# Kernel optimization log

Hardware: AMD Instinct MI355X
Metric: run time of the kernel (lower is better)

Reference implementation:

```python
import jax, jax.numpy as jnp
import numpy as np

N, E, S = 20000, 160000, 3        # nodes, edges, message-passing steps
L, NODE_D, EDGE_D, OUT = 128, 12, 7, 3
LN_EPS = 1e-5


def _mlp(x, W0, b0, W1, b1, W2, b2):
    # Linear -> ReLU -> Linear -> ReLU -> Linear (widths: in->L->L->out)
    h = jax.nn.relu(x @ W0 + b0)
    h = jax.nn.relu(h @ W1 + b1)
    return h @ W2 + b2


def _ln(h, g, b):
    mu = jnp.mean(h, axis=-1, keepdims=True)
    var = jnp.mean((h - mu) ** 2, axis=-1, keepdims=True)
    return (h - mu) * jax.lax.rsqrt(var + LN_EPS) * g + b


def setup_inputs() -> dict:
    ks = iter(jax.random.split(jax.random.key(0), 64))
    w = lambda *s: jax.random.normal(next(ks), s, jnp.float32) * 0.05
    z = lambda *s: jnp.zeros(s, jnp.float32)
    o = lambda *s: jnp.ones(s, jnp.float32)
    inp = {
        'node_x': jax.random.normal(next(ks), (N, NODE_D), jnp.float32),
        'edge_x': jax.random.normal(next(ks), (E, EDGE_D), jnp.float32),
        'enc_n_W0': w(NODE_D, L), 'enc_n_b0': z(L), 'enc_n_W1': w(L, L), 'enc_n_b1': z(L),
        'enc_n_W2': w(L, L), 'enc_n_b2': z(L), 'enc_n_g': o(L), 'enc_n_be': z(L),
        'enc_e_W0': w(EDGE_D, L), 'enc_e_b0': z(L), 'enc_e_W1': w(L, L), 'enc_e_b1': z(L),
        'enc_e_W2': w(L, L), 'enc_e_b2': z(L), 'enc_e_g': o(L), 'enc_e_be': z(L),
        'gnb_e_W0': w(S, 3 * L, L), 'gnb_e_b0': z(S, L), 'gnb_e_W1': w(S, L, L), 'gnb_e_b1': z(S, L),
        'gnb_e_W2': w(S, L, L), 'gnb_e_b2': z(S, L), 'gnb_e_g': o(S, L), 'gnb_e_be': z(S, L),
        'gnb_n_W0': w(S, 2 * L, L), 'gnb_n_b0': z(S, L), 'gnb_n_W1': w(S, L, L), 'gnb_n_b1': z(S, L),
        'gnb_n_W2': w(S, L, L), 'gnb_n_b2': z(S, L), 'gnb_n_g': o(S, L), 'gnb_n_be': z(S, L),
        'dec_W0': w(L, L), 'dec_b0': z(L), 'dec_W1': w(L, L), 'dec_b1': z(L),
        'dec_W2': w(L, OUT), 'dec_b2': z(OUT),
        'senders': jax.random.randint(next(ks), (E,), 0, N, jnp.int32),
        'receivers': jax.random.randint(next(ks), (E,), 0, N, jnp.int32),
    }
    return inp


def reference(node_x, edge_x,
              enc_n_W0, enc_n_b0, enc_n_W1, enc_n_b1, enc_n_W2, enc_n_b2, enc_n_g, enc_n_be,
              enc_e_W0, enc_e_b0, enc_e_W1, enc_e_b1, enc_e_W2, enc_e_b2, enc_e_g, enc_e_be,
              gnb_e_W0, gnb_e_b0, gnb_e_W1, gnb_e_b1, gnb_e_W2, gnb_e_b2, gnb_e_g, gnb_e_be,
              gnb_n_W0, gnb_n_b0, gnb_n_W1, gnb_n_b1, gnb_n_W2, gnb_n_b2, gnb_n_g, gnb_n_be,
              dec_W0, dec_b0, dec_W1, dec_b1, dec_W2, dec_b2,
              senders, receivers):
    num_nodes = node_x.shape[0]
    # Encoder: MLP + LayerNorm on nodes and edges
    nf = _ln(_mlp(node_x, enc_n_W0, enc_n_b0, enc_n_W1, enc_n_b1, enc_n_W2, enc_n_b2), enc_n_g, enc_n_be)
    ef = _ln(_mlp(edge_x, enc_e_W0, enc_e_b0, enc_e_W1, enc_e_b1, enc_e_W2, enc_e_b2), enc_e_g, enc_e_be)

    def step(carry, p):
        nf, ef = carry
        (eW0, eb0, eW1, eb1, eW2, eb2, eg, ebe,
         nW0, nb0, nW1, nb1, nW2, nb2, ng, nbe) = p
        # gather sender/receiver node features -> concat with edge features -> edge MLP
        cat_e = jnp.concatenate([nf[senders], nf[receivers], ef], axis=-1)  # [E, 3L]
        new_ef = _ln(_mlp(cat_e, eW0, eb0, eW1, eb1, eW2, eb2), eg, ebe)
        # scatter-sum updated edge features to receiver nodes
        agg = jax.ops.segment_sum(new_ef, receivers, num_segments=num_nodes)  # [N, L]
        new_nf = _ln(_mlp(jnp.concatenate([nf, agg], axis=-1), nW0, nb0, nW1, nb1, nW2, nb2), ng, nbe)
        # residual connections on both nodes and edges
        return (nf + new_nf, ef + new_ef), None

    step_params = (gnb_e_W0, gnb_e_b0, gnb_e_W1, gnb_e_b1, gnb_e_W2, gnb_e_b2, gnb_e_g, gnb_e_be,
                   gnb_n_W0, gnb_n_b0, gnb_n_W1, gnb_n_b1, gnb_n_W2, gnb_n_b2, gnb_n_g, gnb_n_be)
    (nf, ef), _ = jax.lax.scan(step, (nf, ef), step_params)

    # Decoder: MLP without LayerNorm
    return _mlp(nf, dec_W0, dec_b0, dec_W1, dec_b1, dec_W2, dec_b2)
```

## Files before the change

### kernel.cpp

```cpp
#include <hip/hip_runtime.h>
#include <hip/hip_bf16.h>

#define NN 20000
#define EE 160000

typedef __attribute__((ext_vector_type(8))) short bf16x8;
typedef __attribute__((ext_vector_type(4))) float f32x4;

__device__ __forceinline__ unsigned short f2bf(float f) {
    unsigned int u = __float_as_uint(f);
    u += 0x7FFFu + ((u >> 16) & 1);
    return (unsigned short)(u >> 16);
}
__device__ __forceinline__ float bf2f(short s) {
    return __uint_as_float(((unsigned int)(unsigned short)s) << 16);
}
__device__ __forceinline__ bf16x8 pack8(float4 a, float4 b) {
    bf16x8 r;
    r[0] = (short)f2bf(a.x); r[1] = (short)f2bf(a.y);
    r[2] = (short)f2bf(a.z); r[3] = (short)f2bf(a.w);
    r[4] = (short)f2bf(b.x); r[5] = (short)f2bf(b.y);
    r[6] = (short)f2bf(b.z); r[7] = (short)f2bf(b.w);
    return r;
}

#define SH_STRIDE 136
#define SW_STRIDE 56
#define SH64 132
#define SW64 72

__device__ __forceinline__ void bar_lgkm() {
    asm volatile("s_waitcnt lgkmcnt(0)\n\ts_barrier" ::: "memory");
}

__device__ __forceinline__ void mfma_sweep_lds(f32x4 (&acc)[2][8], bf16x8 a0, bf16x8 a1,
                                               const short* sWb, int lm, int lq)
{
#pragma unroll
    for (int ct = 0; ct < 8; ++ct) {
        bf16x8 b = *(const bf16x8*)(sWb + (ct * 16 + lm) * SW_STRIDE + lq * 8);
        acc[0][ct] = __builtin_amdgcn_mfma_f32_16x16x32_bf16(a0, b, acc[0][ct], 0, 0, 0);
        acc[1][ct] = __builtin_amdgcn_mfma_f32_16x16x32_bf16(a1, b, acc[1][ct], 0, 0, 0);
    }
}

__device__ __forceinline__ void mfma_sweep64(f32x4 (&acc)[2][8], bf16x8 a0, bf16x8 a1,
                                             const short* sWb, int colOff, int lm)
{
#pragma unroll
    for (int ct = 0; ct < 8; ++ct) {
        bf16x8 b = *(const bf16x8*)(sWb + (ct * 16 + lm) * SW64 + colOff);
        acc[0][ct] = __builtin_amdgcn_mfma_f32_16x16x32_bf16(a0, b, acc[0][ct], 0, 0, 0);
        acc[1][ct] = __builtin_amdgcn_mfma_f32_16x16x32_bf16(a1, b, acc[1][ct], 0, 0, 0);
    }
}

__device__ __forceinline__ void mfma_sweepNS(f32x4 (&acc)[4], bf16x8 a,
                                             const short* sWb, int ch, int colOff, int lm)
{
#pragma unroll
    for (int i = 0; i < 4; ++i) {
        int ct = ch * 4 + i;
        bf16x8 b = *(const bf16x8*)(sWb + (ct * 16 + lm) * SW64 + colOff);
        acc[i] = __builtin_amdgcn_mfma_f32_16x16x32_bf16(a, b, acc[i], 0, 0, 0);
    }
}

template<int NT>
struct WStage { bf16x8 v[512 / NT]; };

template<int NT>
__device__ __forceinline__ void wload(WStage<NT>& ws, const short* __restrict__ Wt,
                                      int Kpad, int k0, int tid)
{
#pragma unroll
    for (int j = 0; j < 256 / NT; ++j) {
        int i = tid + j * NT;
        int r = i >> 1, h = i & 1;
        const short* src = Wt + (size_t)r * Kpad + k0 + h * 16;
        ws.v[2 * j]     = *(const bf16x8*)src;
        ws.v[2 * j + 1] = *(const bf16x8*)(src + 8);
    }
}
template<int NT>
__device__ __forceinline__ void wstore(const WStage<NT>& ws, short* __restrict__ sW, int tid)
{
#pragma unroll
    for (int j = 0; j < 256 / NT; ++j) {
        int i = tid + j * NT;
        int r = i >> 1, h = i & 1;
        short* dst = sW + r * SW_STRIDE + h * 16;
        *(bf16x8*)dst       = ws.v[2 * j];
        *(bf16x8*)(dst + 8) = ws.v[2 * j + 1];
    }
}

struct WStage64 { bf16x8 v[4]; };
__device__ __forceinline__ void wload64(WStage64& ws, const short* __restrict__ Wt,
                                        int Kpad, int k0, int tid)
{
#pragma unroll
    for (int j = 0; j < 4; ++j) {
        int i = tid + j * 256;
        int r = i >> 3, h = i & 7;
        ws.v[j] = *(const bf16x8*)(Wt + (size_t)r * Kpad + k0 + h * 8);
    }
}
__device__ __forceinline__ void wstore64(const WStage64& ws, short* __restrict__ sW, int tid)
{
#pragma unroll
    for (int j = 0; j < 4; ++j) {
        int i = tid + j * 256;
        int r = i >> 3, h = i & 7;
        *(bf16x8*)(sW + r * SW64 + h * 8) = ws.v[j];
    }
}

__device__ __forceinline__ void zero_acc(f32x4 (&acc)[2][8]) {
#pragma unroll
    for (int i = 0; i < 2; ++i)
#pragma unroll
        for (int j = 0; j < 8; ++j) acc[i][j] = (f32x4)(0.f);
}

__device__ __forceinline__ void park(const f32x4 (&acc)[2][8], const float* __restrict__ bias,
                                     short* __restrict__ sH, int w32, int lm, int lq)
{
#pragma unroll
    for (int ct = 0; ct < 8; ++ct) {
        float bb = bias[ct * 16 + lm];
#pragma unroll
        for (int rt = 0; rt < 2; ++rt) {
            int rbase = w32 + rt * 16 + lq * 4;
#pragma unroll
            for (int reg = 0; reg < 4; ++reg) {
                float v = fmaxf(acc[rt][ct][reg] + bb, 0.f);
                sH[(rbase + reg) * SH_STRIDE + ct * 16 + lm] = (short)f2bf(v);
            }
        }
    }
}

__device__ __forceinline__ void parkNS(const f32x4 (&acc)[4], const float* __restrict__ bias,
                                       short* __restrict__ sH, int g16, int ch, int lm, int lq)
{
#pragma unroll
    for (int i = 0; i < 4; ++i) {
        int ct = ch * 4 + i;
        float bb = bias[ct * 16 + lm];
#pragma unroll
        for (int reg = 0; reg < 4; ++reg) {
            float v = fmaxf(acc[i][reg] + bb, 0.f);
            sH[(g16 + lq * 4 + reg) * SH_STRIDE + ct * 16 + lm] = (short)f2bf(v);
        }
    }
}

__device__ __forceinline__ void park64(const f32x4 (&acc)[2][8], const float* __restrict__ bias,
                                       short* __restrict__ sH, int w32, int lm, int lq)
{
#pragma unroll
    for (int ct = 0; ct < 8; ++ct) {
        float bb = bias[ct * 16 + lm];
#pragma unroll
        for (int rt = 0; rt < 2; ++rt) {
            int rbase = w32 + rt * 16 + lq * 4;
#pragma unroll
            for (int reg = 0; reg < 4; ++reg) {
                float v = fmaxf(acc[rt][ct][reg] + bb, 0.f);
                sH[(rbase + reg) * SH64 + ct * 16 + lm] = (short)f2bf(v);
            }
        }
    }
}

struct Frag {
    bf16x8 a0, a1;
    float4 f0, f1, f2, f3;
    int isF;
};

template<int MODE>
__device__ __forceinline__ void load_frag(Frag& fr, int c,
    const short* __restrict__ nfb, const float* __restrict__ aggf,
    int r0m, int r1m, const short* sH, int w32, int lm, int lq)
{
    int kq = lq * 8;
    fr.isF = 0;
    if (MODE == 0) {
        fr.a0 = *(const bf16x8*)&sH[(w32 + lm) * SH_STRIDE + c * 32 + kq];
        fr.a1 = *(const bf16x8*)&sH[(w32 + 16 + lm) * SH_STRIDE + c * 32 + kq];
    } else if (MODE == 2) {
        int seg = c >> 2, kb = (c & 3) * 32 + kq;
        if (seg == 0) {
            fr.a0 = *(const bf16x8*)(nfb + (size_t)r0m * 128 + kb);
            fr.a1 = *(const bf16x8*)(nfb + (size_t)r1m * 128 + kb);
        } else {
            const float* p0 = aggf + (size_t)r0m * 128 + kb;
            const float* p1 = aggf + (size_t)r1m * 128 + kb;
            fr.f0 = *(const float4*)p0; fr.f1 = *(const float4*)(p0 + 4);
            fr.f2 = *(const float4*)p1; fr.f3 = *(const float4*)(p1 + 4);
            fr.isF = 1;
        }
    } else {
        int kb = c * 32 + kq;
        fr.a0 = *(const bf16x8*)(nfb + (size_t)r0m * 128 + kb);
        fr.a1 = *(const bf16x8*)(nfb + (size_t)r1m * 128 + kb);
    }
}

template<int MODE>
__device__ __forceinline__ void load_fragNS(Frag& fr, int c,
    const short* __restrict__ nfb, const float* __restrict__ aggf, int r0m, int lq)
{
    fr.isF = 0;
    if (MODE == 2 && c >= 2) {
        const float* p = aggf + (size_t)r0m * 128 + (c - 2) * 64 + lq * 8;
        fr.f0 = *(const float4*)p;        fr.f1 = *(const float4*)(p + 4);
        fr.f2 = *(const float4*)(p + 32); fr.f3 = *(const float4*)(p + 36);
        fr.isF = 1;
    } else {
        const short* p = nfb + (size_t)r0m * 128 + c * 64 + lq * 8;
        fr.a0 = *(const bf16x8*)p;
        fr.a1 = *(const bf16x8*)(p + 32);
    }
}

struct Frag64 { bf16x8 a[4]; };

__device__ __forceinline__ void load_frag64(Frag64& fr, int c,
    const short* __restrict__ nfb, const short* __restrict__ efHi,
    int iS0, int iS1, int iR0, int iR1, size_t eO0, size_t eO1, int lq)
{
    int kb = (c & 1) * 64 + lq * 8;
    int seg = c >> 1;
    const short *base0, *base1;
    if (seg == 0)      { base0 = nfb + (size_t)iS0 * 128; base1 = nfb + (size_t)iS1 * 128; }
    else if (seg == 1) { base0 = nfb + (size_t)iR0 * 128; base1 = nfb + (size_t)iR1 * 128; }
    else               { base0 = efHi + eO0;              base1 = efHi + eO1; }
    fr.a[0] = *(const bf16x8*)(base0 + kb);
    fr.a[1] = *(const bf16x8*)(base1 + kb);
    fr.a[2] = *(const bf16x8*)(base0 + kb + 32);
    fr.a[3] = *(const bf16x8*)(base1 + kb + 32);
}

template<int RESID>
__global__ __launch_bounds__(256) void gnn_edge64(
    const short* __restrict__ Wt0,
    const short* __restrict__ Wt1, const short* __restrict__ Wt2,
    const float* __restrict__ b0, const float* __restrict__ b1, const float* __restrict__ b2,
    const float* __restrict__ g, const float* __restrict__ be,
    const short* __restrict__ nfb,
    short* __restrict__ efHi, short* __restrict__ efLo,
    const int* __restrict__ eList,
    const int* __restrict__ senders, const int* __restrict__ receivers,
    float* __restrict__ aggOut)
{
    __shared__ short sH[128 * SH64];
    __shared__ short sW[128 * SW64];
    __shared__ int sRcv[128], sSnd[128];
    const int tid = threadIdx.x;
    const int lane = tid & 63;
    const int w = tid >> 6;
    const int lm = lane & 15;
    const int lq = lane >> 4;
    const int w32 = w * 32;
    const int m0 = blockIdx.x * 128;

    if (tid < 128) {
        int slot = m0 + tid;
        int e = eList ? eList[slot] : slot;
        sRcv[tid] = receivers[e];
        sSnd[tid] = senders[e];
    }
    bar_lgkm();

    f32x4 acc[2][8];
    zero_acc(acc);

    const int s0 = w32 + 2 * lm, s1 = s0 + 1;
    const int iS0 = sSnd[s0], iS1 = sSnd[s1];
    const int iR0 = sRcv[s0], iR1 = sRcv[s1];
    const size_t eO0 = (size_t)(m0 + s0) * 128;
    const size_t eO1 = (size_t)(m0 + s1) * 128;

    {
        WStage64 ws, wsn;
        Frag64 cur, nxt;
        wload64(ws, Wt0, 384, 0, tid);
        load_frag64(cur, 0, nfb, efHi, iS0, iS1, iR0, iR1, eO0, eO1, lq);
#pragma unroll
        for (int c = 0; c < 6; ++c) {
            if (c + 1 < 6) {
                wload64(wsn, Wt0, 384, (c + 1) * 64, tid);
                load_frag64(nxt, c + 1, nfb, efHi, iS0, iS1, iR0, iR1, eO0, eO1, lq);
            }
            bar_lgkm();
            wstore64(ws, sW, tid);
            bar_lgkm();
            mfma_sweep64(acc, cur.a[0], cur.a[1], sW, lq * 8, lm);
            mfma_sweep64(acc, cur.a[2], cur.a[3], sW, 32 + lq * 8, lm);
            ws = wsn; cur = nxt;
        }
    }
    bar_lgkm();
    park64(acc, b0, sH, w32, lm, lq);

    zero_acc(acc);
    {
        WStage64 ws, wsn;
        wload64(ws, Wt1, 128, 0, tid);
#pragma unroll
        for (int c = 0; c < 2; ++c) {
            if (c == 0) wload64(wsn, Wt1, 128, 64, tid);
            bf16x8 a0h0 = *(const bf16x8*)&sH[(w32 + lm) * SH64 + c * 64 + lq * 8];
            bf16x8 a1h0 = *(const bf16x8*)&sH[(w32 + 16 + lm) * SH64 + c * 64 + lq * 8];
            bf16x8 a0h1 = *(const bf16x8*)&sH[(w32 + lm) * SH64 + c * 64 + 32 + lq * 8];
            bf16x8 a1h1 = *(const bf16x8*)&sH[(w32 + 16 + lm) * SH64 + c * 64 + 32 + lq * 8];
            bar_lgkm();
            wstore64(ws, sW, tid);
            bar_lgkm();
            mfma_sweep64(acc, a0h0, a1h0, sW, lq * 8, lm);
            mfma_sweep64(acc, a0h1, a1h1, sW, 32 + lq * 8, lm);
            ws = wsn;
        }
    }
    bar_lgkm();
    park64(acc, b1, sH, w32, lm, lq);

    zero_acc(acc);
    {
        WStage64 ws, wsn;
        wload64(ws, Wt2, 128, 0, tid);
#pragma unroll
        for (int c = 0; c < 2; ++c) {
            if (c == 0) wload64(wsn, Wt2, 128, 64, tid);
            bf16x8 a0h0 = *(const bf16x8*)&sH[(w32 + lm) * SH64 + c * 64 + lq * 8];
            bf16x8 a1h0 = *(const bf16x8*)&sH[(w32 + 16 + lm) * SH64 + c * 64 + lq * 8];
            bf16x8 a0h1 = *(const bf16x8*)&sH[(w32 + lm) * SH64 + c * 64 + 32 + lq * 8];
            bf16x8 a1h1 = *(const bf16x8*)&sH[(w32 + 16 + lm) * SH64 + c * 64 + 32 + lq * 8];
            bar_lgkm();
            wstore64(ws, sW, tid);
            bar_lgkm();
            mfma_sweep64(acc, a0h0, a1h0, sW, lq * 8, lm);
            mfma_sweep64(acc, a0h1, a1h1, sW, 32 + lq * 8, lm);
            ws = wsn;
        }
    }

    float g_[8], be_[8], b2_[8];
#pragma unroll
    for (int ct = 0; ct < 8; ++ct) {
        g_[ct] = g[ct * 16 + lm]; be_[ct] = be[ct * 16 + lm]; b2_[ct] = b2[ct * 16 + lm];
    }
    float run[8];
    int curRcv = -1;
#pragma unroll
    for (int j = 0; j < 8; ++j) {
        int rt = j & 1, reg = j >> 1;
        int rloc = w32 + lq * 8 + j;
        float v[8];
        float s = 0.f;
#pragma unroll
        for (int ct = 0; ct < 8; ++ct) { v[ct] = acc[rt][ct][reg] + b2_[ct]; s += v[ct]; }
        s += __shfl_xor(s, 1); s += __shfl_xor(s, 2);
        s += __shfl_xor(s, 4); s += __shfl_xor(s, 8);
        float mu = s * (1.f / 128.f);
        float q = 0.f;
#pragma unroll
        for (int ct = 0; ct < 8; ++ct) { v[ct] -= mu; q += v[ct] * v[ct]; }
        q += __shfl_xor(q, 1); q += __shfl_xor(q, 2);
        q += __shfl_xor(q, 4); q += __shfl_xor(q, 8);
        float rs = rsqrtf(q * (1.f / 128.f) + 1e-5f);
        int rcv = sRcv[rloc];
        float o[8];
#pragma unroll
        for (int ct = 0; ct < 8; ++ct) {
            o[ct] = v[ct] * rs * g_[ct] + be_[ct];
            if (RESID) {
                size_t gi = (size_t)(m0 + rloc) * 128 + ct * 16 + lm;
                float x = bf2f(efHi[gi]) + bf2f(efLo[gi]) + o[ct];
                short h = (short)f2bf(x);
                efHi[gi] = h;
                efLo[gi] = (short)f2bf(x - bf2f(h));
            }
        }
        if (rcv != curRcv) {
            if (curRcv >= 0) {
#pragma unroll
                for (int ct = 0; ct < 8; ++ct)
                    atomicAdd(aggOut + (size_t)curRcv * 128 + ct * 16 + lm, run[ct]);
            }
            curRcv = rcv;
#pragma unroll
            for (int ct = 0; ct < 8; ++ct) run[ct] = o[ct];
        } else {
#pragma unroll
            for (int ct = 0; ct < 8; ++ct) run[ct] += o[ct];
        }
    }
    if (curRcv >= 0) {
#pragma unroll
        for (int ct = 0; ct < 8; ++ct)
            atomicAdd(aggOut + (size_t)curRcv * 128 + ct * 16 + lm, run[ct]);
    }
}

template<int NW, int MODE, int PAIR>
__global__ __launch_bounds__(NW * 64) void gnn_mlp(
    const short* __restrict__ Wt0,
    const short* __restrict__ Wt1, const short* __restrict__ Wt2,
    const float* __restrict__ b0, const float* __restrict__ b1, const float* __restrict__ b2,
    const float* __restrict__ g, const float* __restrict__ be,
    const float* __restrict__ A0f, int K0,
    const short* __restrict__ nfb,
    const float* __restrict__ aggf,
    const int* __restrict__ eList,
    float* __restrict__ outF, short* __restrict__ outB, short* __restrict__ outB2,
    float* __restrict__ aggOut,
    float* __restrict__ decOut,
    int M, int resid)
{
    constexpr int KP0 = (MODE == 2) ? 256 : (MODE == 3) ? 128 : 32;
    constexpr int nC0 = KP0 / 32;
    __shared__ short sH[NW * 32 * SH_STRIDE];
    __shared__ short sW[128 * SW_STRIDE];
    const int tid = threadIdx.x;
    const int lane = tid & 63;
    const int w = tid >> 6;
    const int lm = lane & 15;
    const int lq = lane >> 4;
    const int w32 = w * 32;
    const int m0 = blockIdx.x * (NW * 32);
    constexpr int NT = NW * 64;

    f32x4 acc[2][8];
    zero_acc(acc);

    if (MODE == 0) {
#pragma unroll
        for (int i = 0; i < 16; ++i) {
            int flat = lane + i * 64;
            int r = flat >> 5, k = flat & 31;
            int row = m0 + w32 + r;
            float v = 0.f;
            if (k < K0 && row < M) {
                int src = eList ? eList[row] : row;
                v = A0f[(size_t)src * K0 + k];
            }
            sH[(w32 + r) * SH_STRIDE + k] = (short)f2bf(v);
        }
    }
    const int r0m = min(m0 + w32 + lm, M - 1);
    const int r1m = min(m0 + w32 + 16 + lm, M - 1);

    {
        WStage<NT> ws, wsn;
        Frag cur, nx1, nx2;
        wload<NT>(ws, Wt0, KP0, 0, tid);
        load_frag<MODE>(cur, 0, nfb, aggf, r0m, r1m, sH, w32, lm, lq);
        if (nC0 > 1)
            load_frag<MODE>(nx1, 1, nfb, aggf, r0m, r1m, sH, w32, lm, lq);
#pragma unroll
        for (int c = 0; c < nC0; ++c) {
            if (c + 1 < nC0)
                wload<NT>(wsn, Wt0, KP0, (c + 1) * 32, tid);
            if (c + 2 < nC0)
                load_frag<MODE>(nx2, c + 2, nfb, aggf, r0m, r1m, sH, w32, lm, lq);
            bar_lgkm();
            wstore<NT>(ws, sW, tid);
            bar_lgkm();
            bf16x8 u0, u1;
            if (cur.isF) { u0 = pack8(cur.f0, cur.f1); u1 = pack8(cur.f2, cur.f3); }
            else         { u0 = cur.a0;               u1 = cur.a1; }
            mfma_sweep_lds(acc, u0, u1, sW, lm, lq);
            ws = wsn; cur = nx1; nx1 = nx2;
        }
    }
    bar_lgkm();
    park(acc, b0, sH, w32, lm, lq);

    zero_acc(acc);
    {
        WStage<NT> ws, wsn;
        wload<NT>(ws, Wt1, 128, 0, tid);
#pragma unroll
        for (int c = 0; c < 4; ++c) {
            if (c + 1 < 4) wload<NT>(wsn, Wt1, 128, (c + 1) * 32, tid);
            bf16x8 a0 = *(const bf16x8*)&sH[(w32 + lm) * SH_STRIDE + c * 32 + lq * 8];
            bf16x8 a1 = *(const bf16x8*)&sH[(w32 + 16 + lm) * SH_STRIDE + c * 32 + lq * 8];
            bar_lgkm();
            wstore<NT>(ws, sW, tid);
            bar_lgkm();
            mfma_sweep_lds(acc, a0, a1, sW, lm, lq);
            ws = wsn;
        }
    }
    bar_lgkm();
    park(acc, b1, sH, w32, lm, lq);

    zero_acc(acc);
    {
        WStage<NT> ws, wsn;
        wload<NT>(ws, Wt2, 128, 0, tid);
#pragma unroll
        for (int c = 0; c < 4; ++c) {
            if (c + 1 < 4) wload<NT>(wsn, Wt2, 128, (c + 1) * 32, tid);
            bf16x8 a0 = *(const bf16x8*)&sH[(w32 + lm) * SH_STRIDE + c * 32 + lq * 8];
            bf16x8 a1 = *(const bf16x8*)&sH[(w32 + 16 + lm) * SH_STRIDE + c * 32 + lq * 8];
            bar_lgkm();
            wstore<NT>(ws, sW, tid);
            bar_lgkm();
            mfma_sweep_lds(acc, a0, a1, sW, lm, lq);
            ws = wsn;
        }
    }

    float g_[8], be_[8], b2_[8];
#pragma unroll
    for (int ct = 0; ct < 8; ++ct) {
        g_[ct] = g[ct * 16 + lm]; be_[ct] = be[ct * 16 + lm]; b2_[ct] = b2[ct * 16 + lm];
    }
#pragma unroll
    for (int rt = 0; rt < 2; ++rt) {
#pragma unroll
        for (int reg = 0; reg < 4; ++reg) {
            int row = m0 + w32 + rt * 16 + lq * 4 + reg;
            float v[8];
            float s = 0.f;
#pragma unroll
            for (int ct = 0; ct < 8; ++ct) { v[ct] = acc[rt][ct][reg] + b2_[ct]; s += v[ct]; }
            s += __shfl_xor(s, 1); s += __shfl_xor(s, 2);
            s += __shfl_xor(s, 4); s += __shfl_xor(s, 8);
            float mu = s * (1.f / 128.f);
            float q = 0.f;
#pragma unroll
            for (int ct = 0; ct < 8; ++ct) { v[ct] -= mu; q += v[ct] * v[ct]; }
            q += __shfl_xor(q, 1); q += __shfl_xor(q, 2);
            q += __shfl_xor(q, 4); q += __shfl_xor(q, 8);
            float rs = rsqrtf(q * (1.f / 128.f) + 1e-5f);
            if (row < M) {
#pragma unroll
                for (int ct = 0; ct < 8; ++ct) {
                    float o = v[ct] * rs * g_[ct] + be_[ct];
                    size_t gi = (size_t)row * 128 + ct * 16 + lm;
                    if (PAIR) {
                        short h = (short)f2bf(o);
                        outB[gi]  = h;
                        outB2[gi] = (short)f2bf(o - bf2f(h));
                    } else {
                        if (resid) {
                            float ns = outF[gi] + o;
                            outF[gi] = ns;
                            if (outB) outB[gi] = (short)f2bf(ns);
                        } else {
                            outF[gi] = o;
                            if (outB) outB[gi] = (short)f2bf(o);
                        }
                    }
                }
            }
        }
    }
}

template<int MODE>
__global__ __launch_bounds__(256) void gnn_mlpNS(
    const short* __restrict__ Wt0,
    const short* __restrict__ Wt1, const short* __restrict__ Wt2,
    const float* __restrict__ b0, const float* __restrict__ b1, const float* __restrict__ b2,
    const float* __restrict__ g, const float* __restrict__ be,
    const float* __restrict__ A0f, int K0,
    const short* __restrict__ nfb,
    const float* __restrict__ aggf,
    float* __restrict__ outF, short* __restrict__ outB,
    float* __restrict__ aggOut,
    float* __restrict__ decOut,
    int M, int resid)
{
    __shared__ short sH[32 * SH_STRIDE];
    __shared__ short sW[128 * SW64];
    __shared__ float sX[2][32];
    __shared__ float sY[2][32];
    const int tid = threadIdx.x;
    const int lane = tid & 63;
    const int w = tid >> 6;
    const int gidx = w >> 1;
    const int ch = w & 1;
    const int lm = lane & 15;
    const int lq = lane >> 4;
    const int g16 = gidx * 16;
    const int m0 = blockIdx.x * 32;
    const int r0m = min(m0 + g16 + lm, M - 1);

    f32x4 acc[4];
#pragma unroll
    for (int i = 0; i < 4; ++i) acc[i] = (f32x4)(0.f);

    if (MODE == 0) {
#pragma unroll
        for (int i = 0; i < 4; ++i) {
            int flat = tid + i * 256;
            int r = flat >> 5, k = flat & 31;
            int row = m0 + r;
            float v = (k < K0 && row < M) ? A0f[(size_t)row * K0 + k] : 0.f;
            sH[r * SH_STRIDE + k] = (short)f2bf(v);
        }
        {
            const short* src = Wt0 + (size_t)(tid >> 1) * 32 + (tid & 1) * 16;
            bf16x8 w0 = *(const bf16x8*)src;
            bf16x8 w1 = *(const bf16x8*)(src + 8);
            bar_lgkm();
            short* dst = sW + (tid >> 1) * SW64 + (tid & 1) * 16;
            *(bf16x8*)dst       = w0;
            *(bf16x8*)(dst + 8) = w1;
            bar_lgkm();
        }
        bf16x8 a0 = *(const bf16x8*)&sH[(g16 + lm) * SH_STRIDE + lq * 8];
        mfma_sweepNS(acc, a0, sW, ch, lq * 8, lm);
    } else {
        constexpr int KP0 = (MODE == 2) ? 256 : 128;
        constexpr int nC0 = KP0 / 64;
        WStage64 ws, wsn;
        Frag cur, nxt;
        wload64(ws, Wt0, KP0, 0, tid);
        load_fragNS<MODE>(cur, 0, nfb, aggf, r0m, lq);
#pragma unroll
        for (int c = 0; c < nC0; ++c) {
            if (c + 1 < nC0) {
                wload64(wsn, Wt0, KP0, (c + 1) * 64, tid);
                load_fragNS<MODE>(nxt, c + 1, nfb, aggf, r0m, lq);
            }
            bar_lgkm();
            wstore64(ws, sW, tid);
            bar_lgkm();
            bf16x8 u0, u1;
            if (cur.isF) { u0 = pack8(cur.f0, cur.f1); u1 = pack8(cur.f2, cur.f3); }
            else         { u0 = cur.a0;                u1 = cur.a1; }
            mfma_sweepNS(acc, u0, sW, ch, lq * 8, lm);
            mfma_sweepNS(acc, u1, sW, ch, 32 + lq * 8, lm);
            ws = wsn; cur = nxt;
        }
    }
    bar_lgkm();
    parkNS(acc, b0, sH, g16, ch, lm, lq);
    bar_lgkm();

    if (MODE == 2 && aggOut) {
#pragma unroll
        for (int i = 0; i < 4; ++i) {
            int idx = tid + i * 256;
            int r = idx >> 5, c4 = idx & 31;
            int row = m0 + r;
            if (row < M)
                *(float4*)(aggOut + (size_t)row * 128 + c4 * 4) = make_float4(0.f, 0.f, 0.f, 0.f);
        }
    }

#pragma unroll
    for (int i = 0; i < 4; ++i) acc[i] = (f32x4)(0.f);
    {
        WStage64 ws, wsn;
        wload64(ws, Wt1, 128, 0, tid);
#pragma unroll
        for (int c = 0; c < 2; ++c) {
            if (c == 0) wload64(wsn, Wt1, 128, 64, tid);
            bf16x8 a0 = *(const bf16x8*)&sH[(g16 + lm) * SH_STRIDE + c * 64 + lq * 8];
            bf16x8 a1 = *(const bf16x8*)&sH[(g16 + lm) * SH_STRIDE + c * 64 + 32 + lq * 8];
            bar_lgkm();
            wstore64(ws, sW, tid);
            bar_lgkm();
            mfma_sweepNS(acc, a0, sW, ch, lq * 8, lm);
            mfma_sweepNS(acc, a1, sW, ch, 32 + lq * 8, lm);
            ws = wsn;
        }
    }
    bar_lgkm();
    parkNS(acc, b1, sH, g16, ch, lm, lq);
    bar_lgkm();

    if (MODE == 3) {
        if (tid < 96) {
            int r = tid / 3, o = tid - r * 3;
            int row = m0 + r;
            if (row < M) {
                float s = b2[o];
#pragma unroll
                for (int kk = 0; kk < 16; ++kk) {
                    bf16x8 h8 = *(const bf16x8*)&sH[r * SH_STRIDE + kk * 8];
#pragma unroll
                    for (int j = 0; j < 8; ++j)
                        s += bf2f(h8[j]) * A0f[(kk * 8 + j) * 3 + o];
                }
                decOut[(size_t)row * 3 + o] = s;
            }
        }
        return;
    }

#pragma unroll
    for (int i = 0; i < 4; ++i) acc[i] = (f32x4)(0.f);
    {
        WStage64 ws, wsn;
        wload64(ws, Wt2, 128, 0, tid);
#pragma unroll
        for (int c = 0; c < 2; ++c) {
            if (c == 0) wload64(wsn, Wt2, 128, 64, tid);
            bf16x8 a0 = *(const bf16x8*)&sH[(g16 + lm) * SH_STRIDE + c * 64 + lq * 8];
            bf16x8 a1 = *(const bf16x8*)&sH[(g16 + lm) * SH_STRIDE + c * 64 + 32 + lq * 8];
            bar_lgkm();
            wstore64(ws, sW, tid);
            bar_lgkm();
            mfma_sweepNS(acc, a0, sW, ch, lq * 8, lm);
            mfma_sweepNS(acc, a1, sW, ch, 32 + lq * 8, lm);
            ws = wsn;
        }
    }

    float g_[4], be_[4], b2_[4];
#pragma unroll
    for (int i = 0; i < 4; ++i) {
        int ct = ch * 4 + i;
        g_[i] = g[ct * 16 + lm]; be_[i] = be[ct * 16 + lm]; b2_[i] = b2[ct * 16 + lm];
    }
    float v[4][4], mu[4], rs_[4];
#pragma unroll
    for (int reg = 0; reg < 4; ++reg) {
        float s = 0.f;
#pragma unroll
        for (int i = 0; i < 4; ++i) { v[i][reg] = acc[i][reg] + b2_[i]; s += v[i][reg]; }
        s += __shfl_xor(s, 1); s += __shfl_xor(s, 2);
        s += __shfl_xor(s, 4); s += __shfl_xor(s, 8);
        if (lm == 0) sX[ch][g16 + lq * 4 + reg] = s;
    }
    bar_lgkm();
#pragma unroll
    for (int reg = 0; reg < 4; ++reg)
        mu[reg] = (sX[0][g16 + lq * 4 + reg] + sX[1][g16 + lq * 4 + reg]) * (1.f / 128.f);
#pragma unroll
    for (int reg = 0; reg < 4; ++reg) {
        float q = 0.f;
#pragma unroll
        for (int i = 0; i < 4; ++i) { v[i][reg] -= mu[reg]; q += v[i][reg] * v[i][reg]; }
        q += __shfl_xor(q, 1); q += __shfl_xor(q, 2);
        q += __shfl_xor(q, 4); q += __shfl_xor(q, 8);
        if (lm == 0) sY[ch][g16 + lq * 4 + reg] = q;
    }
    bar_lgkm();
#pragma unroll
    for (int reg = 0; reg < 4; ++reg)
        rs_[reg] = rsqrtf((sY[0][g16 + lq * 4 + reg] + sY[1][g16 + lq * 4 + reg]) * (1.f / 128.f) + 1e-5f);
#pragma unroll
    for (int reg = 0; reg < 4; ++reg) {
        int row = m0 + g16 + lq * 4 + reg;
        if (row < M) {
#pragma unroll
            for (int i = 0; i < 4; ++i) {
                float o = v[i][reg] * rs_[reg] * g_[i] + be_[i];
                size_t gi = (size_t)row * 128 + (size_t)(ch * 4 + i) * 16 + lm;
                if (resid) {
                    float ns = outF[gi] + o;
                    outF[gi] = ns;
                    if (outB) outB[gi] = (short)f2bf(ns);
                } else {
                    outF[gi] = o;
                    if (outB) outB[gi] = (short)f2bf(o);
                }
            }
        }
    }
}

__global__ void zero_i(int* __restrict__ p, int n)
{
    int i = blockIdx.x * 256 + threadIdx.x;
    if (i < n) p[i] = 0;
}
__global__ void csr_count(const int* __restrict__ recv, int* __restrict__ cnt, int E)
{
    int i = blockIdx.x * 256 + threadIdx.x;
    if (i < E) atomicAdd(&cnt[recv[i]], 1);
}
__global__ __launch_bounds__(256) void csr_scan(const int* __restrict__ cnt,
                                                int* __restrict__ cursor, int N)
{
    __shared__ int ssum[257];
    const int tid = threadIdx.x;
    const int per = (N + 255) / 256;
    const int lo = tid * per, hi = min(lo + per, N);
    int s = 0;
    for (int i = lo; i < hi; ++i) s += cnt[i];
    ssum[tid] = s;
    __syncthreads();
    if (tid == 0) {
        int run = 0;
        for (int i = 0; i < 256; ++i) { int t = ssum[i]; ssum[i] = run; run += t; }
        ssum[256] = run;
    }
    __syncthreads();
    int run = ssum[tid];
    for (int i = lo; i < hi; ++i) { int c = cnt[i]; cursor[i] = run; run += c; }
}
__global__ void csr_fill(const int* __restrict__ recv, int* __restrict__ cursor,
                         int* __restrict__ eList, int E)
{
    int i = blockIdx.x * 256 + threadIdx.x;
    if (i < E) {
        int pos = atomicAdd(&cursor[recv[i]], 1);
        eList[pos] = i;
    }
}

struct WtPrep { const float* src; int K; int Kpad; int dstOff; };
struct WtPrepAll { WtPrep m[26]; };

__global__ void wt_prep_kernel(WtPrepAll all, short* __restrict__ dst)
{
    const WtPrep p = all.m[blockIdx.y];
    int total = 128 * p.Kpad;
    int idx = blockIdx.x * 256 + threadIdx.x;
    if (idx >= total) return;
    int n = idx / p.Kpad, k = idx - n * p.Kpad;
    float v = (k < p.K) ? p.src[(size_t)k * 128 + n] : 0.f;
    dst[p.dstOff + idx] = (short)f2bf(v);
}

__global__ void zero_kernel(float4* __restrict__ p, long n4)
{
    long i = (long)blockIdx.x * blockDim.x + threadIdx.x;
    if (i < n4) p[i] = make_float4(0.f, 0.f, 0.f, 0.f);
}

extern "C" void kernel_launch(void* const* d_in, const int* in_sizes, int n_in,
                              void* d_out, int out_size, void* d_ws, size_t ws_size,
                              hipStream_t stream)
{
    const float* node_x   = (const float*)d_in[0];
    const float* edge_x   = (const float*)d_in[1];
    const float* enc_n_W0 = (const float*)d_in[2];
    const float* enc_n_b0 = (const float*)d_in[3];
    const float* enc_n_W1 = (const float*)d_in[4];
    const float* enc_n_b1 = (const float*)d_in[5];
    const float* enc_n_W2 = (const float*)d_in[6];
    const float* enc_n_b2 = (const float*)d_in[7];
    const float* enc_n_g  = (const float*)d_in[8];
    const float* enc_n_be = (const float*)d_in[9];
    const float* enc_e_W0 = (const float*)d_in[10];
    const float* enc_e_b0 = (const float*)d_in[11];
    const float* enc_e_W1 = (const float*)d_in[12];
    const float* enc_e_b1 = (const float*)d_in[13];
    const float* enc_e_W2 = (const float*)d_in[14];
    const float* enc_e_b2 = (const float*)d_in[15];
    const float* enc_e_g  = (const float*)d_in[16];
    const float* enc_e_be = (const float*)d_in[17];
    const float* gnb_e_W0 = (const float*)d_in[18];
    const float* gnb_e_b0 = (const float*)d_in[19];
    const float* gnb_e_W1 = (const float*)d_in[20];
    const float* gnb_e_b1 = (const float*)d_in[21];
    const float* gnb_e_W2 = (const float*)d_in[22];
    const float* gnb_e_b2 = (const float*)d_in[23];
    const float* gnb_e_g  = (const float*)d_in[24];
    const float* gnb_e_be = (const float*)d_in[25];
    const float* gnb_n_W0 = (const float*)d_in[26];
    const float* gnb_n_b0 = (const float*)d_in[27];
    const float* gnb_n_W1 = (const float*)d_in[28];
    const float* gnb_n_b1 = (const float*)d_in[29];
    const float* gnb_n_W2 = (const float*)d_in[30];
    const float* gnb_n_b2 = (const float*)d_in[31];
    const float* gnb_n_g  = (const float*)d_in[32];
    const float* gnb_n_be = (const float*)d_in[33];
    const float* dec_W0   = (const float*)d_in[34];
    const float* dec_b0   = (const float*)d_in[35];
    const float* dec_W1   = (const float*)d_in[36];
    const float* dec_b1   = (const float*)d_in[37];
    const float* dec_W2   = (const float*)d_in[38];
    const float* dec_b2   = (const float*)d_in[39];
    const int*   senders  = (const int*)d_in[40];
    const int*   receivers= (const int*)d_in[41];
    float* out = (float*)d_out;

    const int N = NN, E = EE;
    const int WT_TOTAL = (32 + 128 + 128 + 32 + 128 + 128 + 3 * (384 + 128 + 128 + 256 + 128 + 128)
                          + 128 + 128) * 128;

    float* nf   = (float*)d_ws;
    float* agg  = nf + (size_t)N * 128;
    short* efHi = (short*)(agg + (size_t)N * 128);
    short* efLo = efHi + (size_t)E * 128;
    short* nfbf = efLo + (size_t)E * 128;
    short* wt   = nfbf + (size_t)N * 128;
    int*   eList = (int*)(wt + WT_TOTAL);
    size_t need_sorted = (size_t)((char*)(eList + E) - (char*)d_ws);
    int* cnt    = (int*)agg;
    int* cursor = cnt + N;

    const bool useSorted = (ws_size >= need_sorted);
    const int* eL = useSorted ? eList : nullptr;

    WtPrepAll tbl;
    int nMat = 0, off = 0;
    int o_encn[3], o_ence[3], o_ge0[3], o_ge1[3], o_ge2[3], o_gn0[3], o_gn1[3], o_gn2[3], o_dec[2];
    auto add = [&](const float* src, int K, int Kpad) {
        tbl.m[nMat].src = src; tbl.m[nMat].K = K; tbl.m[nMat].Kpad = Kpad;
        tbl.m[nMat].dstOff = off;
        int r = off; off += 128 * Kpad; ++nMat; return r;
    };
    o_encn[0] = add(enc_n_W0, 12, 32);
    o_encn[1] = add(enc_n_W1, 128, 128);
    o_encn[2] = add(enc_n_W2, 128, 128);
    o_ence[0] = add(enc_e_W0, 7, 32);
    o_ence[1] = add(enc_e_W1, 128, 128);
    o_ence[2] = add(enc_e_W2, 128, 128);
    for (int s = 0; s < 3; ++s) {
        o_ge0[s] = add(gnb_e_W0 + (size_t)s * 384 * 128, 384, 384);
        o_ge1[s] = add(gnb_e_W1 + (size_t)s * 128 * 128, 128, 128);
        o_ge2[s] = add(gnb_e_W2 + (size_t)s * 128 * 128, 128, 128);
        o_gn0[s] = add(gnb_n_W0 + (size_t)s * 256 * 128, 256, 256);
        o_gn1[s] = add(gnb_n_W1 + (size_t)s * 128 * 128, 128, 128);
        o_gn2[s] = add(gnb_n_W2 + (size_t)s * 128 * 128, 128, 128);
    }
    o_dec[0] = add(dec_W0, 128, 128);
    o_dec[1] = add(dec_W1, 128, 128);

    wt_prep_kernel<<<dim3(192, 26), 256, 0, stream>>>(tbl, wt);

    if (useSorted) {
        zero_i<<<dim3((N + 255) / 256), 256, 0, stream>>>(cnt, N);
        csr_count<<<dim3((E + 255) / 256), 256, 0, stream>>>(receivers, cnt, E);
        csr_scan<<<dim3(1), 256, 0, stream>>>(cnt, cursor, N);
        csr_fill<<<dim3((E + 255) / 256), 256, 0, stream>>>(receivers, cursor, eList, E);
    }
    zero_kernel<<<dim3((N * 32 + 255) / 256), 256, 0, stream>>>((float4*)agg, (long)N * 32);

    const dim3 gE(E / 128);
    const dim3 gNS(N / 32);

    gnn_mlpNS<0><<<gNS, 256, 0, stream>>>(wt + o_encn[0], wt + o_encn[1], wt + o_encn[2],
        enc_n_b0, enc_n_b1, enc_n_b2, enc_n_g, enc_n_be,
        node_x, 12, nullptr, nullptr,
        nf, nfbf, nullptr, nullptr, N, 0);
    gnn_mlp<4, 0, 1><<<gE, 256, 0, stream>>>(wt + o_ence[0], wt + o_ence[1], wt + o_ence[2],
        enc_e_b0, enc_e_b1, enc_e_b2, enc_e_g, enc_e_be,
        edge_x, 7, nullptr, nullptr, eL,
        nullptr, efHi, efLo, nullptr, nullptr, E, 0);

    for (int s = 0; s < 3; ++s) {
        const float* eb0 = gnb_e_b0 + (size_t)s * 128;
        const float* eb1 = gnb_e_b1 + (size_t)s * 128;
        const float* eb2 = gnb_e_b2 + (size_t)s * 128;
        const float* eg  = gnb_e_g  + (size_t)s * 128;
        const float* ebe = gnb_e_be + (size_t)s * 128;
        const float* nb0 = gnb_n_b0 + (size_t)s * 128;
        const float* nb1 = gnb_n_b1 + (size_t)s * 128;
        const float* nb2 = gnb_n_b2 + (size_t)s * 128;
        const float* ng  = gnb_n_g  + (size_t)s * 128;
        const float* nbe = gnb_n_be + (size_t)s * 128;

        if (s < 2) {
            gnn_edge64<1><<<gE, 256, 0, stream>>>(wt + o_ge0[s], wt + o_ge1[s], wt + o_ge2[s],
                eb0, eb1, eb2, eg, ebe,
                nfbf, efHi, efLo, eL, senders, receivers, agg);
        } else {
            gnn_edge64<0><<<gE, 256, 0, stream>>>(wt + o_ge0[s], wt + o_ge1[s], wt + o_ge2[s],
                eb0, eb1, eb2, eg, ebe,
                nfbf, efHi, efLo, eL, senders, receivers, agg);
        }
        gnn_mlpNS<2><<<gNS, 256, 0, stream>>>(wt + o_gn0[s], wt + o_gn1[s], wt + o_gn2[s],
            nb0, nb1, nb2, ng, nbe,
            nullptr, 0, nfbf, agg,
            nf, nfbf, agg, nullptr, N, 1);
    }

    gnn_mlpNS<3><<<gNS, 256, 0, stream>>>(wt + o_dec[0], wt + o_dec[1], nullptr,
        dec_b0, dec_b1, dec_b2, nullptr, nullptr,
        dec_W2, 0, nfbf, nullptr,
        nullptr, nullptr, nullptr, out, N, 0);
}
```

Measured before the change: 563.8 us.

## Split edge MLP tile across 8 waves with 16 rows each

The edge MLP kernel now launches 512 threads per 128-edge block, so each wave handles 16 edges instead of 32. Accumulators shrink from 2x8 to 8 MFMA tiles and weight staging is spread over twice as many threads. The aim is more waves in flight per block and lower per-thread register pressure, improving latency hiding for the gathers. In exchange each weight B-fragment read from LDS now feeds only one MFMA instead of two, and barriers synchronise more waves. The edge-ordering mapping for the scatter/LN epilogue is changed as well, which could affect correctness if other code assumed the old row mapping.

```diff
diff --git a/kernel.cpp b/kernel.cpp
--- a/kernel.cpp
+++ b/kernel.cpp
@@ -44,14 +44,13 @@
     }
 }
 
-__device__ __forceinline__ void mfma_sweep64(f32x4 (&acc)[2][8], bf16x8 a0, bf16x8 a1,
+__device__ __forceinline__ void mfma_sweep16(f32x4 (&acc)[8], bf16x8 a,
                                              const short* sWb, int colOff, int lm)
 {
 #pragma unroll
     for (int ct = 0; ct < 8; ++ct) {
         bf16x8 b = *(const bf16x8*)(sWb + (ct * 16 + lm) * SW64 + colOff);
-        acc[0][ct] = __builtin_amdgcn_mfma_f32_16x16x32_bf16(a0, b, acc[0][ct], 0, 0, 0);
-        acc[1][ct] = __builtin_amdgcn_mfma_f32_16x16x32_bf16(a1, b, acc[1][ct], 0, 0, 0);
+        acc[ct] = __builtin_amdgcn_mfma_f32_16x16x32_bf16(a, b, acc[ct], 0, 0, 0);
     }
 }
 
@@ -95,22 +94,26 @@
     }
 }
 
-struct WStage64 { bf16x8 v[4]; };
-__device__ __forceinline__ void wload64(WStage64& ws, const short* __restrict__ Wt,
+template<int NT>
+struct WStage64 { bf16x8 v[1024 / NT]; };
+
+template<int NT>
+__device__ __forceinline__ void wload64(WStage64<NT>& ws, const short* __restrict__ Wt,
                                         int Kpad, int k0, int tid)
 {
 #pragma unroll
-    for (int j = 0; j < 4; ++j) {
-        int i = tid + j * 256;
+    for (int j = 0; j < 1024 / NT; ++j) {
+        int i = tid + j * NT;
         int r = i >> 3, h = i & 7;
         ws.v[j] = *(const bf16x8*)(Wt + (size_t)r * Kpad + k0 + h * 8);
     }
 }
-__device__ __forceinline__ void wstore64(const WStage64& ws, short* __restrict__ sW, int tid)
-{
-#pragma unroll
-    for (int j = 0; j < 4; ++j) {
-        int i = tid + j * 256;
+template<int NT>
+__device__ __forceinline__ void wstore64(const WStage64<NT>& ws, short* __restrict__ sW, int tid)
+{
+#pragma unroll
+    for (int j = 0; j < 1024 / NT; ++j) {
+        int i = tid + j * NT;
         int r = i >> 3, h = i & 7;
         *(bf16x8*)(sW + r * SW64 + h * 8) = ws.v[j];
     }
@@ -121,6 +124,10 @@
     for (int i = 0; i < 2; ++i)
 #pragma unroll
         for (int j = 0; j < 8; ++j) acc[i][j] = (f32x4)(0.f);
+}
+__device__ __forceinline__ void zero_acc8(f32x4 (&acc)[8]) {
+#pragma unroll
+    for (int j = 0; j < 8; ++j) acc[j] = (f32x4)(0.f);
 }
 
 __device__ __forceinline__ void park(const f32x4 (&acc)[2][8], const float* __restrict__ bias,
@@ -156,20 +163,17 @@
     }
 }
 
-__device__ __forceinline__ void park64(const f32x4 (&acc)[2][8], const float* __restrict__ bias,
-                                       short* __restrict__ sH, int w32, int lm, int lq)
+__device__ __forceinline__ void park16e(const f32x4 (&acc)[8], const float* __restrict__ bias,
+                                        short* __restrict__ sH, int w16, int lm, int lq)
 {
 #pragma unroll
     for (int ct = 0; ct < 8; ++ct) {
         float bb = bias[ct * 16 + lm];
-#pragma unroll
-        for (int rt = 0; rt < 2; ++rt) {
-            int rbase = w32 + rt * 16 + lq * 4;
-#pragma unroll
-            for (int reg = 0; reg < 4; ++reg) {
-                float v = fmaxf(acc[rt][ct][reg] + bb, 0.f);
-                sH[(rbase + reg) * SH64 + ct * 16 + lm] = (short)f2bf(v);
-            }
+        int rbase = w16 + lq * 4;
+#pragma unroll
+        for (int reg = 0; reg < 4; ++reg) {
+            float v = fmaxf(acc[ct][reg] + bb, 0.f);
+            sH[(rbase + reg) * SH64 + ct * 16 + lm] = (short)f2bf(v);
         }
     }
 }
@@ -226,26 +230,24 @@
     }
 }
 
-struct Frag64 { bf16x8 a[4]; };
-
-__device__ __forceinline__ void load_frag64(Frag64& fr, int c,
+struct Frag64h { bf16x8 a[2]; };
+
+__device__ __forceinline__ void load_frag64h(Frag64h& fr, int c,
     const short* __restrict__ nfb, const short* __restrict__ efHi,
-    int iS0, int iS1, int iR0, int iR1, size_t eO0, size_t eO1, int lq)
+    int iS0, int iR0, size_t eO0, int lq)
 {
     int kb = (c & 1) * 64 + lq * 8;
     int seg = c >> 1;
-    const short *base0, *base1;
-    if (seg == 0)      { base0 = nfb + (size_t)iS0 * 128; base1 = nfb + (size_t)iS1 * 128; }
-    else if (seg == 1) { base0 = nfb + (size_t)iR0 * 128; base1 = nfb + (size_t)iR1 * 128; }
-    else               { base0 = efHi + eO0;              base1 = efHi + eO1; }
-    fr.a[0] = *(const bf16x8*)(base0 + kb);
-    fr.a[1] = *(const bf16x8*)(base1 + kb);
-    fr.a[2] = *(const bf16x8*)(base0 + kb + 32);
-    fr.a[3] = *(const bf16x8*)(base1 + kb + 32);
+    const short* base;
+    if (seg == 0)      base = nfb + (size_t)iS0 * 128;
+    else if (seg == 1) base = nfb + (size_t)iR0 * 128;
+    else               base = efHi + eO0;
+    fr.a[0] = *(const bf16x8*)(base + kb);
+    fr.a[1] = *(const bf16x8*)(base + kb + 32);
 }
 
 template<int RESID>
-__global__ __launch_bounds__(256) void gnn_edge64(
+__global__ __launch_bounds__(512) void gnn_edge64(
     const short* __restrict__ Wt0,
     const short* __restrict__ Wt1, const short* __restrict__ Wt2,
     const float* __restrict__ b0, const float* __restrict__ b1, const float* __restrict__ b2,
@@ -264,7 +266,7 @@
     const int w = tid >> 6;
     const int lm = lane & 15;
     const int lq = lane >> 4;
-    const int w32 = w * 32;
+    const int w16 = w * 16;
     const int m0 = blockIdx.x * 128;
 
     if (tid < 128) {
@@ -275,75 +277,70 @@
     }
     bar_lgkm();
 
-    f32x4 acc[2][8];
-    zero_acc(acc);
-
-    const int s0 = w32 + 2 * lm, s1 = s0 + 1;
-    const int iS0 = sSnd[s0], iS1 = sSnd[s1];
-    const int iR0 = sRcv[s0], iR1 = sRcv[s1];
+    f32x4 acc[8];
+    zero_acc8(acc);
+
+    const int s0 = w16 + lm;
+    const int iS0 = sSnd[s0];
+    const int iR0 = sRcv[s0];
     const size_t eO0 = (size_t)(m0 + s0) * 128;
-    const size_t eO1 = (size_t)(m0 + s1) * 128;
 
     {
-        WStage64 ws, wsn;
-        Frag64 cur, nxt;
-        wload64(ws, Wt0, 384, 0, tid);
-        load_frag64(cur, 0, nfb, efHi, iS0, iS1, iR0, iR1, eO0, eO1, lq);
+        WStage64<512> ws, wsn;
+        Frag64h cur, nxt;
+        wload64<512>(ws, Wt0, 384, 0, tid);
+        load_frag64h(cur, 0, nfb, efHi, iS0, iR0, eO0, lq);
 #pragma unroll
         for (int c = 0; c < 6; ++c) {
             if (c + 1 < 6) {
-                wload64(wsn, Wt0, 384, (c + 1) * 64, tid);
-                load_frag64(nxt, c + 1, nfb, efHi, iS0, iS1, iR0, iR1, eO0, eO1, lq);
+                wload64<512>(wsn, Wt0, 384, (c + 1) * 64, tid);
+                load_frag64h(nxt, c + 1, nfb, efHi, iS0, iR0, eO0, lq);
             }
             bar_lgkm();
-            wstore64(ws, sW, tid);
-            bar_lgkm();
-            mfma_sweep64(acc, cur.a[0], cur.a[1], sW, lq * 8, lm);
-            mfma_sweep64(acc, cur.a[2], cur.a[3], sW, 32 + lq * 8, lm);
+            wstore64<512>(ws, sW, tid);
+            bar_lgkm();
+            mfma_sweep16(acc, cur.a[0], sW, lq * 8, lm);
+            mfma_sweep16(acc, cur.a[1], sW, 32 + lq * 8, lm);
             ws = wsn; cur = nxt;
         }
     }
     bar_lgkm();
-    park64(acc, b0, sH, w32, lm, lq);
-
-    zero_acc(acc);
+    park16e(acc, b0, sH, w16, lm, lq);
+
+    zero_acc8(acc);
     {
-        WStage64 ws, wsn;
-        wload64(ws, Wt1, 128, 0, tid);
+        WStage64<512> ws, wsn;
+        wload64<512>(ws, Wt1, 128, 0, tid);
 #pragma unroll
         for (int c = 0; c < 2; ++c) {
-            if (c == 0) wload64(wsn, Wt1, 128, 64, tid);
-            bf16x8 a0h0 = *(const bf16x8*)&sH[(w32 + lm) * SH64 + c * 64 + lq * 8];
-            bf16x8 a1h0 = *(const bf16x8*)&sH[(w32 + 16 + lm) * SH64 + c * 64 + lq * 8];
-            bf16x8 a0h1 = *(const bf16x8*)&sH[(w32 + lm) * SH64 + c * 64 + 32 + lq * 8];
-            bf16x8 a1h1 = *(const bf16x8*)&sH[(w32 + 16 + lm) * SH64 + c * 64 + 32 + lq * 8];
-            bar_lgkm();
-            wstore64(ws, sW, tid);
-            bar_lgkm();
-            mfma_sweep64(acc, a0h0, a1h0, sW, lq * 8, lm);
-            mfma_sweep64(acc, a0h1, a1h1, sW, 32 + lq * 8, lm);
+            if (c == 0) wload64<512>(wsn, Wt1, 128, 64, tid);
+            bf16x8 a0 = *(const bf16x8*)&sH[(w16 + lm) * SH64 + c * 64 + lq * 8];
+            bf16x8 a1 = *(const bf16x8*)&sH[(w16 + lm) * SH64 + c * 64 + 32 + lq * 8];
+            bar_lgkm();
+            wstore64<512>(ws, sW, tid);
+            bar_lgkm();
+            mfma_sweep16(acc, a0, sW, lq * 8, lm);
+            mfma_sweep16(acc, a1, sW, 32 + lq * 8, lm);
             ws = wsn;
         }
     }
     bar_lgkm();
-    park64(acc, b1, sH, w32, lm, lq);
-
-    zero_acc(acc);
+    park16e(acc, b1, sH, w16, lm, lq);
+
+    zero_acc8(acc);
     {
-        WStage64 ws, wsn;
-        wload64(ws, Wt2, 128, 0, tid);
+        WStage64<512> ws, wsn;
+        wload64<512>(ws, Wt2, 128, 0, tid);
 #pragma unroll
         for (int c = 0; c < 2; ++c) {
-            if (c == 0) wload64(wsn, Wt2, 128, 64, tid);
-            bf16x8 a0h0 = *(const bf16x8*)&sH[(w32 + lm) * SH64 + c * 64 + lq * 8];
-            bf16x8 a1h0 = *(const bf16x8*)&sH[(w32 + 16 + lm) * SH64 + c * 64 + lq * 8];
-            bf16x8 a0h1 = *(const bf16x8*)&sH[(w32 + lm) * SH64 + c * 64 + 32 + lq * 8];
-            bf16x8 a1h1 = *(const bf16x8*)&sH[(w32 + 16 + lm) * SH64 + c * 64 + 32 + lq * 8];
-            bar_lgkm();
-            wstore64(ws, sW, tid);
-            bar_lgkm();
-            mfma_sweep64(acc, a0h0, a1h0, sW, lq * 8, lm);
-            mfma_sweep64(acc, a0h1, a1h1, sW, 32 + lq * 8, lm);
+            if (c == 0) wload64<512>(wsn, Wt2, 128, 64, tid);
+            bf16x8 a0 = *(const bf16x8*)&sH[(w16 + lm) * SH64 + c * 64 + lq * 8];
+            bf16x8 a1 = *(const bf16x8*)&sH[(w16 + lm) * SH64 + c * 64 + 32 + lq * 8];
+            bar_lgkm();
+            wstore64<512>(ws, sW, tid);
+            bar_lgkm();
+            mfma_sweep16(acc, a0, sW, lq * 8, lm);
+            mfma_sweep16(acc, a1, sW, 32 + lq * 8, lm);
             ws = wsn;
         }
     }
@@ -356,13 +353,12 @@
     float run[8];
     int curRcv = -1;
 #pragma unroll
-    for (int j = 0; j < 8; ++j) {
-        int rt = j & 1, reg = j >> 1;
-        int rloc = w32 + lq * 8 + j;
+    for (int reg = 0; reg < 4; ++reg) {
+        int rloc = w16 + lq * 4 + reg;
         float v[8];
         float s = 0.f;
 #pragma unroll
-        for (int ct = 0; ct < 8; ++ct) { v[ct] = acc[rt][ct][reg] + b2_[ct]; s += v[ct]; }
+        for (int ct = 0; ct < 8; ++ct) { v[ct] = acc[ct][reg] + b2_[ct]; s += v[ct]; }
         s += __shfl_xor(s, 1); s += __shfl_xor(s, 2);
         s += __shfl_xor(s, 4); s += __shfl_xor(s, 8);
         float mu = s * (1.f / 128.f);
@@ -621,18 +617,18 @@
     } else {
         constexpr int KP0 = (MODE == 2) ? 256 : 128;
         constexpr int nC0 = KP0 / 64;
-        WStage64 ws, wsn;
+        WStage64<256> ws, wsn;
         Frag cur, nxt;
-        wload64(ws, Wt0, KP0, 0, tid);
+        wload64<256>(ws, Wt0, KP0, 0, tid);
         load_fragNS<MODE>(cur, 0, nfb, aggf, r0m, lq);
 #pragma unroll
         for (int c = 0; c < nC0; ++c) {
             if (c + 1 < nC0) {
-                wload64(wsn, Wt0, KP0, (c + 1) * 64, tid);
+                wload64<256>(wsn, Wt0, KP0, (c + 1) * 64, tid);
                 load_fragNS<MODE>(nxt, c + 1, nfb, aggf, r0m, lq);
             }
             bar_lgkm();
-            wstore64(ws, sW, tid);
+            wstore64<256>(ws, sW, tid);
             bar_lgkm();
             bf16x8 u0, u1;
             if (cur.isF) { u0 = pack8(cur.f0, cur.f1); u1 = pack8(cur.f2, cur.f3); }
@@ -660,15 +656,15 @@
 #pragma unroll
     for (int i = 0; i < 4; ++i) acc[i] = (f32x4)(0.f);
     {
-        WStage64 ws, wsn;
-        wload64(ws, Wt1, 128, 0, tid);
+        WStage64<256> ws, wsn;
+        wload64<256>(ws, Wt1, 128, 0, tid);
 #pragma unroll
         for (int c = 0; c < 2; ++c) {
-            if (c == 0) wload64(wsn, Wt1, 128, 64, tid);
+            if (c == 0) wload64<256>(wsn, Wt1, 128, 64, tid);
             bf16x8 a0 = *(const bf16x8*)&sH[(g16 + lm) * SH_STRIDE + c * 64 + lq * 8];
             bf16x8 a1 = *(const bf16x8*)&sH[(g16 + lm) * SH_STRIDE + c * 64 + 32 + lq * 8];
             bar_lgkm();
-            wstore64(ws, sW, tid);
+            wstore64<256>(ws, sW, tid);
             bar_lgkm();
             mfma_sweepNS(acc, a0, sW, ch, lq * 8, lm);
             mfma_sweepNS(acc, a1, sW, ch, 32 + lq * 8, lm);
@@ -701,15 +697,15 @@
 #pragma unroll
     for (int i = 0; i < 4; ++i) acc[i] = (f32x4)(0.f);
     {
-        WStage64 ws, wsn;
-        wload64(ws, Wt2, 128, 0, tid);
+        WStage64<256> ws, wsn;
+        wload64<256>(ws, Wt2, 128, 0, tid);
 #pragma unroll
         for (int c = 0; c < 2; ++c) {
-            if (c == 0) wload64(wsn, Wt2, 128, 64, tid);
+            if (c == 0) wload64<256>(wsn, Wt2, 128, 64, tid);
             bf16x8 a0 = *(const bf16x8*)&sH[(g16 + lm) * SH_STRIDE + c * 64 + lq * 8];
             bf16x8 a1 = *(const bf16x8*)&sH[(g16 + lm) * SH_STRIDE + c * 64 + 32 + lq * 8];
             bar_lgkm();
-            wstore64(ws, sW, tid);
+            wstore64<256>(ws, sW, tid);
             bar_lgkm();
             mfma_sweepNS(acc, a0, sW, ch, lq * 8, lm);
             mfma_sweepNS(acc, a1, sW, ch, 32 + lq * 8, lm);
@@ -957,11 +953,11 @@
         const float* nbe = gnb_n_be + (size_t)s * 128;
 
         if (s < 2) {
-            gnn_edge64<1><<<gE, 256, 0, stream>>>(wt + o_ge0[s], wt + o_ge1[s], wt + o_ge2[s],
+            gnn_edge64<1><<<gE, 512, 0, stream>>>(wt + o_ge0[s], wt + o_ge1[s], wt + o_ge2[s],
                 eb0, eb1, eb2, eg, ebe,
                 nfbf, efHi, efLo, eL, senders, receivers, agg);
         } else {
-            gnn_edge64<0><<<gE, 256, 0, stream>>>(wt + o_ge0[s], wt + o_ge1[s], wt + o_ge2[s],
+            gnn_edge64<0><<<gE, 512, 0, stream>>>(wt + o_ge0[s], wt + o_ge1[s], wt + o_ge2[s],
                 eb0, eb1, eb2, eg, ebe,
                 nfbf, efHi, efLo, eL, senders, receivers, agg);
         }
```

New measurement: 608.3 us. +7.9%, slower.
